# Performance work log

Hardware: AMD Instinct MI355X
Metric: run time of the kernel (lower is better)

Reference implementation:

```python
import jax, jax.numpy as jnp
import numpy as np
import math

B, C, H, W = 16, 256, 128, 128
N = 4096
D = 256  # out_channels
IMG = 512


def _bilinear_sample(features, grid):
    """features (B,C,H,W), grid (B,N,2) in [-1,1] (x,y). align_corners=True, border padding."""
    Bq, Cq, Hq, Wq = features.shape
    ix = (grid[..., 0] + 1.0) * 0.5 * (Wq - 1)  # (B,N)
    iy = (grid[..., 1] + 1.0) * 0.5 * (Hq - 1)
    # border padding: clamp continuous coords into valid range
    ix = jnp.clip(ix, 0.0, Wq - 1)
    iy = jnp.clip(iy, 0.0, Hq - 1)
    x0 = jnp.floor(ix)
    y0 = jnp.floor(iy)
    wx = ix - x0
    wy = iy - y0
    x0i = jnp.clip(x0.astype(jnp.int32), 0, Wq - 1)
    y0i = jnp.clip(y0.astype(jnp.int32), 0, Hq - 1)
    x1i = jnp.clip(x0i + 1, 0, Wq - 1)
    y1i = jnp.clip(y0i + 1, 0, Hq - 1)
    f = features.reshape(Bq, Cq, Hq * Wq)

    def gather(yi, xi):
        idx = (yi * Wq + xi)[:, None, :]  # (B,1,N)
        return jnp.take_along_axis(f, idx, axis=2)  # (B,C,N)

    v00 = gather(y0i, x0i)
    v01 = gather(y0i, x1i)
    v10 = gather(y1i, x0i)
    v11 = gather(y1i, x1i)
    wx = wx[:, None, :]
    wy = wy[:, None, :]
    top = v00 * (1 - wx) + v01 * wx
    bot = v10 * (1 - wx) + v11 * wx
    return top * (1 - wy) + bot * wy  # (B,C,N)


def _pos_encoding(positions, d_model):
    """positions (B,N,2) in [0,1] -> (B,N,2*d_model) sinusoidal."""
    div_term = jnp.exp(jnp.arange(0, d_model, 2, dtype=jnp.float32)
                       * (-math.log(10000.0) / d_model))  # (d_model//2,)
    x = positions[..., 0:1] * 1000.0  # (B,N,1)
    y = positions[..., 1:2] * 1000.0

    def interleave(v):
        a = v * div_term  # (B,N,d_model//2)
        sc = jnp.stack([jnp.sin(a), jnp.cos(a)], axis=-1)  # (B,N,d//2,2)
        return sc.reshape(*v.shape[:-1], d_model)

    return jnp.concatenate([interleave(x), interleave(y)], axis=-1)


def setup_inputs() -> dict:
    key = jax.random.key(0)
    ks = jax.random.split(key, 8)
    features = jax.random.normal(ks[0], (B, C, H, W), dtype=jnp.float32)
    vertices = jax.random.uniform(ks[1], (B, N, 2), dtype=jnp.float32) * IMG
    s1 = 1.0 / math.sqrt(C)
    s2 = 1.0 / math.sqrt(D)
    W1 = jax.random.uniform(ks[2], (C, D), jnp.float32, -s1, s1)
    b1 = jnp.zeros((D,), jnp.float32)
    W2 = jax.random.uniform(ks[3], (D, D), jnp.float32, -s2, s2)
    b2 = jnp.zeros((D,), jnp.float32)
    Wp = jax.random.uniform(ks[4], (D, D), jnp.float32, -s2, s2)
    bp = jnp.zeros((D,), jnp.float32)
    return {"features": features, "vertices": vertices, "image_size": IMG,
            "W1": W1, "b1": b1, "W2": W2, "b2": b2, "Wp": Wp, "bp": bp}


def reference(features, vertices, image_size, W1, b1, W2, b2, Wp, bp):
    # normalize pixel coords to [-1,1] (align_corners=True convention)
    denom = jnp.float32(image_size - 1)
    grid = 2.0 * vertices / denom - 1.0  # (B,N,2)
    sampled = _bilinear_sample(features, grid)  # (B,C,N)
    sampled = jnp.transpose(sampled, (0, 2, 1))  # (B,N,C)
    h = jax.nn.relu(jnp.einsum('bnc,cd->bnd', sampled, W1) + b1)
    vfeat = jnp.einsum('bnd,de->bne', h, W2) + b2  # (B,N,D)
    pos_enc = _pos_encoding(vertices / jnp.float32(image_size), D // 2)  # (B,N,D)
    out = jnp.einsum('bnd,de->bne', vfeat + pos_enc, Wp) + bp
    return out
```

## Files before the change

### kernel.cpp

```cpp
#include <hip/hip_runtime.h>

#define HW 16384
#define Nn 4096

typedef __bf16 bf16x8 __attribute__((ext_vector_type(8)));
typedef unsigned short us8t __attribute__((ext_vector_type(8)));
typedef float f32x4 __attribute__((ext_vector_type(4)));
typedef unsigned int u32x4 __attribute__((ext_vector_type(4)));

__device__ __forceinline__ unsigned short f2bf(float f) {
    unsigned int u = __float_as_uint(f);
    u = (u + 0x7fffu + ((u >> 16) & 1u)) >> 16;
    return (unsigned short)u;
}
__device__ __forceinline__ float bf2f(unsigned int h) {
    return __uint_as_float(h << 16);
}
__device__ __forceinline__ unsigned int pack2bf(float lo, float hi) {
    const unsigned int u0 = __float_as_uint(lo) + 0x8000u;
    const unsigned int u1 = __float_as_uint(hi) + 0x8000u;
    return __builtin_amdgcn_perm(u1, u0, 0x07060302u);
}
__device__ __forceinline__ f32x4 mfma16(us8t a, us8t b, f32x4 c) {
    return __builtin_amdgcn_mfma_f32_16x16x32_bf16(
        __builtin_bit_cast(bf16x8, a), __builtin_bit_cast(bf16x8, b), c, 0, 0, 0);
}

__global__ __launch_bounds__(256) void k_wt(const float* __restrict__ W1,
                                            const float* __restrict__ W2,
                                            const float* __restrict__ Wp,
                                            unsigned short* __restrict__ WT) {
    const int m = blockIdx.x >> 8;
    const int d = blockIdx.x & 255;
    const int c = threadIdx.x;
    const float* W = (m == 0) ? W1 : (m == 1) ? W2 : Wp;
    WT[m * 65536 + d * 256 + c] = f2bf(W[c * 256 + d]);
}

__global__ __launch_bounds__(256) void k_pix(const float* __restrict__ f,
                                             const unsigned short* __restrict__ W1T,
                                             unsigned short* __restrict__ S, int b0) {
    __shared__ __align__(16) unsigned int Asb[64 * 132];

    const int blk = blockIdx.x;
    const int bl = blk >> 8;
    const int b = b0 + bl;
    const int p0 = (blk & 255) << 6;
    const int t = threadIdx.x;
    const int lane = t & 63;
    const int w = t >> 6;
    const int mrow = lane & 15;
    const int kg = (lane >> 4) << 3;

    const float* fb = f + ((size_t)b << 22);

    const int sp = (t & 15) << 2;
    const int c8 = (t >> 4) << 3;
#pragma unroll
    for (int pass = 0; pass < 2; ++pass) {
        const int c0 = c8 + (pass << 7);
        f32x4 v[8];
#pragma unroll
        for (int i = 0; i < 8; ++i)
            v[i] = *(const f32x4*)(fb + ((size_t)(c0 + i) << 14) + p0 + sp);
#pragma unroll
        for (int j = 0; j < 4; ++j) {
            u32x4 pk;
            pk.x = pack2bf(v[0][j], v[1][j]);
            pk.y = pack2bf(v[2][j], v[3][j]);
            pk.z = pack2bf(v[4][j], v[5][j]);
            pk.w = pack2bf(v[6][j], v[7][j]);
            *(u32x4*)&Asb[(sp + j) * 132 + (c0 >> 1)] = pk;
        }
    }

    f32x4 acc[4][4];
#pragma unroll
    for (int i = 0; i < 4; ++i)
#pragma unroll
        for (int j = 0; j < 4; ++j) acc[i][j] = (f32x4){0.f, 0.f, 0.f, 0.f};

    const unsigned short* AW = W1T + (((w << 6) + mrow) << 8) + kg;
    us8t aN[4];
#pragma unroll
    for (int mt = 0; mt < 4; ++mt) aN[mt] = *(const us8t*)(AW + (mt << 12));

    __syncthreads();

    const unsigned short* Bl = (const unsigned short*)Asb + mrow * 264 + kg;
#pragma unroll
    for (int k0 = 0; k0 < 256; k0 += 32) {
        us8t aC[4];
#pragma unroll
        for (int mt = 0; mt < 4; ++mt) aC[mt] = aN[mt];
        if (k0 < 224) {
#pragma unroll
            for (int mt = 0; mt < 4; ++mt)
                aN[mt] = *(const us8t*)(AW + (mt << 12) + k0 + 32);
        }
        us8t bF[4];
#pragma unroll
        for (int nt = 0; nt < 4; ++nt)
            bF[nt] = *(const us8t*)(Bl + nt * 16 * 264 + k0);
#pragma unroll
        for (int mt = 0; mt < 4; ++mt)
#pragma unroll
            for (int nt = 0; nt < 4; ++nt)
                acc[mt][nt] = mfma16(aC[mt], bF[nt], acc[mt][nt]);
    }

    unsigned short* Sp = S + ((((size_t)bl << 14) + p0 + mrow) << 8) + (w << 6) + ((lane >> 4) << 2);
#pragma unroll
    for (int nt = 0; nt < 4; ++nt) {
        unsigned short* Sr = Sp + ((size_t)(nt << 4) << 8);
#pragma unroll
        for (int mt = 0; mt < 4; ++mt) {
            uint2 pk;
            pk.x = pack2bf(acc[mt][nt][0], acc[mt][nt][1]);
            pk.y = pack2bf(acc[mt][nt][2], acc[mt][nt][3]);
            *(uint2*)(Sr + (mt << 4)) = pk;
        }
    }
}

__global__ __launch_bounds__(256) void k_gather(const unsigned short* __restrict__ S,
                                                const float* __restrict__ verts,
                                                const int* __restrict__ iszp,
                                                const float* __restrict__ b1,
                                                unsigned short* __restrict__ h, int b0) {
    const int t = threadIdx.x;
    const int lane = t & 63;
    const int w = t >> 6;
    const int blk = blockIdx.x;
    const int bl = blk >> 10;
    const int n = ((blk & 1023) << 2) + w;
    const int b = b0 + bl;

    const float isz = (float)iszp[0];
    const size_t vo = ((size_t)b * Nn + n) << 1;
    const float vx = verts[vo];
    const float vy = verts[vo + 1];
    const float gs = 127.0f / (isz - 1.0f);
    const float ix = fminf(fmaxf(vx * gs, 0.0f), 127.0f);
    const float iy = fminf(fmaxf(vy * gs, 0.0f), 127.0f);
    const float x0 = floorf(ix), y0 = floorf(iy);
    const float wx = ix - x0, wy = iy - y0;
    const int x0i = (int)x0, y0i = (int)y0;
    const int x1i = min(x0i + 1, 127), y1i = min(y0i + 1, 127);
    const float w00 = (1.0f - wx) * (1.0f - wy);
    const float w01 = wx * (1.0f - wy);
    const float w10 = (1.0f - wx) * wy;
    const float w11 = wx * wy;

    const unsigned short* Sb = S + ((size_t)bl << 22);
    const int co = lane << 2;
    const uint2 a0 = *(const uint2*)(Sb + (((size_t)(y0i << 7) + x0i) << 8) + co);
    const uint2 a1 = *(const uint2*)(Sb + (((size_t)(y0i << 7) + x1i) << 8) + co);
    const uint2 a2 = *(const uint2*)(Sb + (((size_t)(y1i << 7) + x0i) << 8) + co);
    const uint2 a3 = *(const uint2*)(Sb + (((size_t)(y1i << 7) + x1i) << 8) + co);
    const float4 bb = *(const float4*)(b1 + co);

    float d0 = w00 * bf2f(a0.x & 0xffffu) + w01 * bf2f(a1.x & 0xffffu) +
               w10 * bf2f(a2.x & 0xffffu) + w11 * bf2f(a3.x & 0xffffu) + bb.x;
    float d1 = w00 * bf2f(a0.x >> 16) + w01 * bf2f(a1.x >> 16) +
               w10 * bf2f(a2.x >> 16) + w11 * bf2f(a3.x >> 16) + bb.y;
    float d2 = w00 * bf2f(a0.y & 0xffffu) + w01 * bf2f(a1.y & 0xffffu) +
               w10 * bf2f(a2.y & 0xffffu) + w11 * bf2f(a3.y & 0xffffu) + bb.z;
    float d3 = w00 * bf2f(a0.y >> 16) + w01 * bf2f(a1.y >> 16) +
               w10 * bf2f(a2.y >> 16) + w11 * bf2f(a3.y >> 16) + bb.w;
    d0 = fmaxf(d0, 0.0f);
    d1 = fmaxf(d1, 0.0f);
    d2 = fmaxf(d2, 0.0f);
    d3 = fmaxf(d3, 0.0f);
    uint2 pk;
    pk.x = pack2bf(d0, d1);
    pk.y = pack2bf(d2, d3);
    *(uint2*)(h + (((size_t)bl * Nn + n) << 8) + co) = pk;
}

__global__ __launch_bounds__(256) void k_mlp(const unsigned short* __restrict__ h,
                                             const float* __restrict__ verts,
                                             const int* __restrict__ iszp,
                                             const unsigned short* __restrict__ W2T,
                                             const unsigned short* __restrict__ WpT,
                                             const float* __restrict__ b2,
                                             const float* __restrict__ bpv,
                                             float* __restrict__ out, int b0) {
    __shared__ __align__(16) unsigned short gT[64][264];
    __shared__ float vps[64][2];
    __shared__ float b2s[256], bps[256];

    const int blk = blockIdx.x;
    const int bl = blk >> 6;
    const int b = b0 + bl;
    const int n0 = (blk & 63) << 6;
    const int t = threadIdx.x;
    const int lane = t & 63;
    const int w = t >> 6;

    b2s[t] = b2[t];
    bps[t] = bpv[t];
    if (t < 64) {
        const float isz = (float)iszp[0];
        const size_t vo = ((size_t)b * Nn + n0 + t) << 1;
        vps[t][0] = verts[vo] / isz;
        vps[t][1] = verts[vo + 1] / isz;
    }

    const int mrow = lane & 15;
    const int kg = (lane >> 4) << 3;
    const int r0 = (lane >> 4) << 2;
    const int n0w = w << 6;

    const unsigned short* hb = h + (((size_t)bl * Nn + n0 + mrow) << 8) + kg;
    const unsigned short* B2 = W2T + ((n0w + mrow) << 8) + kg;
    f32x4 acc[4][4];
#pragma unroll
    for (int i = 0; i < 4; ++i)
#pragma unroll
        for (int j = 0; j < 4; ++j) acc[i][j] = (f32x4){0.f, 0.f, 0.f, 0.f};

    us8t aN[4], bN[4];
#pragma unroll
    for (int mt = 0; mt < 4; ++mt) aN[mt] = *(const us8t*)(hb + (mt << 12));
#pragma unroll
    for (int nt = 0; nt < 4; ++nt) bN[nt] = *(const us8t*)(B2 + (nt << 12));
#pragma unroll
    for (int k0 = 0; k0 < 256; k0 += 32) {
        us8t aC[4], bC[4];
#pragma unroll
        for (int i = 0; i < 4; ++i) { aC[i] = aN[i]; bC[i] = bN[i]; }
        if (k0 < 224) {
#pragma unroll
            for (int mt = 0; mt < 4; ++mt) aN[mt] = *(const us8t*)(hb + (mt << 12) + k0 + 32);
#pragma unroll
            for (int nt = 0; nt < 4; ++nt) bN[nt] = *(const us8t*)(B2 + (nt << 12) + k0 + 32);
        }
#pragma unroll
        for (int mt = 0; mt < 4; ++mt)
#pragma unroll
            for (int nt = 0; nt < 4; ++nt)
                acc[mt][nt] = mfma16(aC[mt], bC[nt], acc[mt][nt]);
    }
    __syncthreads();

    const float C2 = -0.20762050593046f;
#pragma unroll
    for (int nt = 0; nt < 4; ++nt) {
        const int col = n0w + (nt << 4) + mrow;
        const float bias2 = b2s[col];
        const int ci = col & 127;
        const float dv = exp2f((float)(ci >> 1) * C2) * 1000.0f;
        const int sel = col >> 7;
#pragma unroll
        for (int mt = 0; mt < 4; ++mt)
#pragma unroll
            for (int j = 0; j < 4; ++j) {
                const int row = (mt << 4) + r0 + j;
                const float ang = vps[row][sel] * dv;
                const float pe = (col & 1) ? __cosf(ang) : __sinf(ang);
                const float val = acc[mt][nt][j] + bias2 + pe;
                gT[row][col] = (unsigned short)((__float_as_uint(val) + 0x8000u) >> 16);
            }
    }
    __syncthreads();

#pragma unroll
    for (int i = 0; i < 4; ++i)
#pragma unroll
        for (int j = 0; j < 4; ++j) acc[i][j] = (f32x4){0.f, 0.f, 0.f, 0.f};
    const unsigned short* Bp = WpT + ((n0w + mrow) << 8) + kg;
#pragma unroll
    for (int nt = 0; nt < 4; ++nt) bN[nt] = *(const us8t*)(Bp + (nt << 12));
    const unsigned short* Al = &gT[mrow][kg];
#pragma unroll
    for (int k0 = 0; k0 < 256; k0 += 32) {
        us8t bC[4];
#pragma unroll
        for (int i = 0; i < 4; ++i) bC[i] = bN[i];
        if (k0 < 224) {
#pragma unroll
            for (int nt = 0; nt < 4; ++nt) bN[nt] = *(const us8t*)(Bp + (nt << 12) + k0 + 32);
        }
        us8t aC[4];
#pragma unroll
        for (int mt = 0; mt < 4; ++mt)
            aC[mt] = *(const us8t*)(Al + mt * 16 * 264 + k0);
#pragma unroll
        for (int mt = 0; mt < 4; ++mt)
#pragma unroll
            for (int nt = 0; nt < 4; ++nt)
                acc[mt][nt] = mfma16(aC[mt], bC[nt], acc[mt][nt]);
    }

    float* ob = out + (((size_t)b * Nn + n0) << 8);
#pragma unroll
    for (int nt = 0; nt < 4; ++nt) {
        const int col = n0w + (nt << 4) + mrow;
        const float bb = bps[col];
#pragma unroll
        for (int mt = 0; mt < 4; ++mt)
#pragma unroll
            for (int j = 0; j < 4; ++j) {
                const int row = (mt << 4) + r0 + j;
                ob[((size_t)row << 8) + col] = acc[mt][nt][j] + bb;
            }
    }
}

extern "C" void kernel_launch(void* const* d_in, const int* in_sizes, int n_in,
                              void* d_out, int out_size, void* d_ws, size_t ws_size,
                              hipStream_t stream) {
    const float* f = (const float*)d_in[0];
    const float* verts = (const float*)d_in[1];
    const int* isz = (const int*)d_in[2];
    const float* W1 = (const float*)d_in[3];
    const float* b1 = (const float*)d_in[4];
    const float* W2 = (const float*)d_in[5];
    const float* b2 = (const float*)d_in[6];
    const float* Wp = (const float*)d_in[7];
    const float* bp = (const float*)d_in[8];
    float* out = (float*)d_out;

    unsigned short* WT = (unsigned short*)d_ws;
    const size_t S_OFF = 1u << 20;
    const size_t perS = (size_t)HW * 256 * 2;
    const size_t perH = (size_t)Nn * 256 * 2;
    const size_t avail = (ws_size > S_OFF) ? (ws_size - S_OFF) : 0;
    int nbMax = (int)(avail / (perS + perH));
    if (nbMax < 1) nbMax = 1;
    if (nbMax > 16) nbMax = 16;
    unsigned short* S = (unsigned short*)((char*)d_ws + S_OFF);
    unsigned short* Hb = (unsigned short*)((char*)d_ws + S_OFF + (size_t)nbMax * perS);

    k_wt<<<dim3(768), dim3(256), 0, stream>>>(W1, W2, Wp, WT);
    for (int b0 = 0; b0 < 16; b0 += nbMax) {
        const int nb = (16 - b0 < nbMax) ? (16 - b0) : nbMax;
        k_pix<<<dim3(nb * 256), dim3(256), 0, stream>>>(f, WT, S, b0);
        k_gather<<<dim3(nb * 1024), dim3(256), 0, stream>>>(S, verts, isz, b1, Hb, b0);
        k_mlp<<<dim3(nb * 64), dim3(256), 0, stream>>>(Hb, verts, isz, WT + 65536, WT + 131072,
                                                       b2, bp, out, b0);
    }
}
```

Before: 539.4 us.

## Restructure k_pix into 1024-thread blocks with double-buffered K-slab staging

The per-pixel W1 projection kernel now uses 1024-thread blocks covering 256 pixels, split across 16 waves as 4 D-tiles by 4 pixel-tiles. Instead of loading all 256 channels into LDS up front, it streams 32-channel slabs through two LDS buffers with a padded pitch, issuing the global loads for the next slab while MFMAs run on the current one. The aim is to overlap the feature-map reads with compute and to cut LDS bank conflicts. In exchange there are more barriers, narrower 8-byte global loads, scalar LDS reads for the B fragments, and W1 fragments are reloaded from global memory without prefetch.

```diff
diff --git a/kernel.cpp b/kernel.cpp
--- a/kernel.cpp
+++ b/kernel.cpp
@@ -2,10 +2,12 @@
 
 #define HW 16384
 #define Nn 4096
+#define PITCH 19
 
 typedef __bf16 bf16x8 __attribute__((ext_vector_type(8)));
 typedef unsigned short us8t __attribute__((ext_vector_type(8)));
 typedef float f32x4 __attribute__((ext_vector_type(4)));
+typedef float f32x2 __attribute__((ext_vector_type(2)));
 typedef unsigned int u32x4 __attribute__((ext_vector_type(4)));
 
 __device__ __forceinline__ unsigned short f2bf(float f) {
@@ -37,42 +39,51 @@
     WT[m * 65536 + d * 256 + c] = f2bf(W[c * 256 + d]);
 }
 
-__global__ __launch_bounds__(256) void k_pix(const float* __restrict__ f,
-                                             const unsigned short* __restrict__ W1T,
-                                             unsigned short* __restrict__ S, int b0) {
-    __shared__ __align__(16) unsigned int Asb[64 * 132];
+__global__ __launch_bounds__(1024) void k_pix(const float* __restrict__ f,
+                                              const unsigned short* __restrict__ W1T,
+                                              unsigned short* __restrict__ S, int b0) {
+    __shared__ unsigned int Asb[2][256 * PITCH];
 
     const int blk = blockIdx.x;
-    const int bl = blk >> 8;
+    const int bl = blk >> 6;
     const int b = b0 + bl;
-    const int p0 = (blk & 255) << 6;
+    const int p0 = (blk & 63) << 8;
     const int t = threadIdx.x;
     const int lane = t & 63;
     const int w = t >> 6;
+
+    const float* fb = f + ((size_t)b << 22) + p0;
+
+    const int c4 = (t >> 7) << 2;
+    const int sc2 = (t >> 7) << 1;
+    const int sp = (t & 127) << 1;
+
+    f32x2 vst[2][4];
+
+#define ISSUE(ts, set)                                                            \
+    {                                                                             \
+        const float* fp = fb + ((size_t)(((ts) << 5) + c4) << 14) + sp;           \
+        vst[set][0] = *(const f32x2*)(fp);                                        \
+        vst[set][1] = *(const f32x2*)(fp + (1 << 14));                            \
+        vst[set][2] = *(const f32x2*)(fp + (2 << 14));                            \
+        vst[set][3] = *(const f32x2*)(fp + (3 << 14));                            \
+    }
+
+#define PACKW(ts)                                                                 \
+    {                                                                             \
+        const int set_ = (ts) & 1;                                                \
+        unsigned int* Bf = Asb[(ts) & 1];                                         \
+        _Pragma("unroll") for (int j = 0; j < 2; ++j) {                           \
+            unsigned int* row = Bf + (sp + j) * PITCH + sc2;                      \
+            row[0] = pack2bf(vst[set_][0][j], vst[set_][1][j]);                   \
+            row[1] = pack2bf(vst[set_][2][j], vst[set_][3][j]);                   \
+        }                                                                         \
+    }
+
     const int mrow = lane & 15;
-    const int kg = (lane >> 4) << 3;
-
-    const float* fb = f + ((size_t)b << 22);
-
-    const int sp = (t & 15) << 2;
-    const int c8 = (t >> 4) << 3;
-#pragma unroll
-    for (int pass = 0; pass < 2; ++pass) {
-        const int c0 = c8 + (pass << 7);
-        f32x4 v[8];
-#pragma unroll
-        for (int i = 0; i < 8; ++i)
-            v[i] = *(const f32x4*)(fb + ((size_t)(c0 + i) << 14) + p0 + sp);
-#pragma unroll
-        for (int j = 0; j < 4; ++j) {
-            u32x4 pk;
-            pk.x = pack2bf(v[0][j], v[1][j]);
-            pk.y = pack2bf(v[2][j], v[3][j]);
-            pk.z = pack2bf(v[4][j], v[5][j]);
-            pk.w = pack2bf(v[6][j], v[7][j]);
-            *(u32x4*)&Asb[(sp + j) * 132 + (c0 >> 1)] = pk;
-        }
-    }
+    const int quad = lane >> 4;
+    const int dw = (w & 3) << 6;
+    const int pw = (w >> 2) << 6;
 
     f32x4 acc[4][4];
 #pragma unroll
@@ -80,36 +91,41 @@
 #pragma unroll
         for (int j = 0; j < 4; ++j) acc[i][j] = (f32x4){0.f, 0.f, 0.f, 0.f};
 
-    const unsigned short* AW = W1T + (((w << 6) + mrow) << 8) + kg;
-    us8t aN[4];
-#pragma unroll
-    for (int mt = 0; mt < 4; ++mt) aN[mt] = *(const us8t*)(AW + (mt << 12));
-
+    const unsigned short* AW = W1T + ((dw + mrow) << 8) + (quad << 3);
+
+    ISSUE(0, 0);
+    ISSUE(1, 1);
+    PACKW(0);
     __syncthreads();
 
-    const unsigned short* Bl = (const unsigned short*)Asb + mrow * 264 + kg;
-#pragma unroll
-    for (int k0 = 0; k0 < 256; k0 += 32) {
-        us8t aC[4];
-#pragma unroll
-        for (int mt = 0; mt < 4; ++mt) aC[mt] = aN[mt];
-        if (k0 < 224) {
+#pragma unroll
+    for (int s = 0; s < 8; ++s) {
+        if (s < 6) ISSUE(s + 2, s & 1);
+        us8t afr[4];
+#pragma unroll
+        for (int mt = 0; mt < 4; ++mt)
+            afr[mt] = *(const us8t*)(AW + (mt << 12) + (s << 5));
+        const unsigned int* Bb = Asb[s & 1] + (pw + mrow) * PITCH + (quad << 2);
+#pragma unroll
+        for (int nt = 0; nt < 4; ++nt) {
+            u32x4 tmp;
+            const unsigned int* Br = Bb + nt * 16 * PITCH;
+            tmp.x = Br[0];
+            tmp.y = Br[1];
+            tmp.z = Br[2];
+            tmp.w = Br[3];
+            const us8t bfr = __builtin_bit_cast(us8t, tmp);
 #pragma unroll
             for (int mt = 0; mt < 4; ++mt)
-                aN[mt] = *(const us8t*)(AW + (mt << 12) + k0 + 32);
-        }
-        us8t bF[4];
-#pragma unroll
-        for (int nt = 0; nt < 4; ++nt)
-            bF[nt] = *(const us8t*)(Bl + nt * 16 * 264 + k0);
-#pragma unroll
-        for (int mt = 0; mt < 4; ++mt)
-#pragma unroll
-            for (int nt = 0; nt < 4; ++nt)
-                acc[mt][nt] = mfma16(aC[mt], bF[nt], acc[mt][nt]);
-    }
-
-    unsigned short* Sp = S + ((((size_t)bl << 14) + p0 + mrow) << 8) + (w << 6) + ((lane >> 4) << 2);
+                acc[mt][nt] = mfma16(afr[mt], bfr, acc[mt][nt]);
+        }
+        if (s < 7) {
+            PACKW(s + 1);
+            __syncthreads();
+        }
+    }
+
+    unsigned short* Sp = S + ((((size_t)bl << 14) + p0 + pw + mrow) << 8) + dw + (quad << 2);
 #pragma unroll
     for (int nt = 0; nt < 4; ++nt) {
         unsigned short* Sr = Sp + ((size_t)(nt << 4) << 8);
@@ -121,6 +137,8 @@
             *(uint2*)(Sr + (mt << 4)) = pk;
         }
     }
+#undef ISSUE
+#undef PACKW
 }
 
 __global__ __launch_bounds__(256) void k_gather(const unsigned short* __restrict__ S,
@@ -336,7 +354,7 @@
     k_wt<<<dim3(768), dim3(256), 0, stream>>>(W1, W2, Wp, WT);
     for (int b0 = 0; b0 < 16; b0 += nbMax) {
         const int nb = (16 - b0 < nbMax) ? (16 - b0) : nbMax;
-        k_pix<<<dim3(nb * 256), dim3(256), 0, stream>>>(f, WT, S, b0);
+        k_pix<<<dim3(nb * 64), dim3(1024), 0, stream>>>(f, WT, S, b0);
         k_gather<<<dim3(nb * 1024), dim3(256), 0, stream>>>(S, verts, isz, b1, Hb, b0);
         k_mlp<<<dim3(nb * 64), dim3(256), 0, stream>>>(Hb, verts, isz, WT + 65536, WT + 131072,
                                                        b2, bp, out, b0);
```

New measurement: 529.4 us. About the same (-1.9%).
